# Kernel optimization log

Measured on AMD Instinct MI355X. Metric: run time of the kernel, lower is better.

Reference implementation:

```python
import jax, jax.numpy as jnp
import numpy as np

D_MODEL = 512
TOP_P = 0.25


def setup_inputs() -> dict:
    key = jax.random.key(0)
    ks = jax.random.split(key, 7)
    B, T, D = 4, 4096, D_MODEL
    s = 1.0 / np.sqrt(D)
    return {
        "h": jax.random.normal(ks[0], (B, T, D), dtype=jnp.float32),
        "Wq": jax.random.normal(ks[1], (D, D), dtype=jnp.float32) * s,
        "bq": jnp.zeros((D,), dtype=jnp.float32),
        "Wk": jax.random.normal(ks[2], (D, D), dtype=jnp.float32) * s,
        "bk": jnp.zeros((D,), dtype=jnp.float32),
        "Wv": jax.random.normal(ks[3], (D, D), dtype=jnp.float32) * s,
        "bv": jnp.zeros((D,), dtype=jnp.float32),
    }


def reference(h, Wq, bq, Wk, bk, Wv, bv):
    B, T, D = h.shape
    q = h @ Wq + bq
    k = h @ Wk + bk
    v = h @ Wv + bv
    # [B, T, T] attention scores, scaled by sqrt(d_model)
    scores = jnp.einsum("btd,bsd->bts", q, k) / jnp.sqrt(jnp.asarray(D, h.dtype))
    k_keep = max(1, int(TOP_P * T))
    vals, idx = jax.lax.top_k(scores, k_keep)  # [B, T, k_keep]
    # scatter top-k values back into a -inf-filled mask along the key axis
    bi = jnp.arange(B)[:, None, None]
    ti = jnp.arange(T)[None, :, None]
    mask = jnp.full(scores.shape, -jnp.inf, dtype=scores.dtype)
    mask = mask.at[bi, ti, idx].set(vals)
    attn = jax.nn.softmax(mask, axis=-1)
    out = jnp.einsum("bts,bsd->btd", attn, v)
    return out[:, -1, :]  # only last query's output is used
```

## Files before the change

### kernel.cpp

```cpp
#include <hip/hip_runtime.h>
#include <hip/hip_bf16.h>

#define B 4
#define T 4096
#define D 512
#define KKEEP 1024
#define RSQRT_D 0.044194173824159216f

__device__ __forceinline__ unsigned f2ord(float f) {
    unsigned u = __float_as_uint(f);
    return (u & 0x80000000u) ? ~u : (u | 0x80000000u);
}
__device__ __forceinline__ float ord2f(unsigned o) {
    return __uint_as_float((o & 0x80000000u) ? (o ^ 0x80000000u) : ~o);
}

__global__ void k_zero(float* a, int na, float* o, int no) {
    int i = blockIdx.x * blockDim.x + threadIdx.x;
    if (i < na) a[i] = 0.f;
    if (i < no) o[i] = 0.f;
}

__global__ void k_qlast(const float* __restrict__ h, const float* __restrict__ Wq,
                        const float* __restrict__ bq, float* __restrict__ qlast) {
    int b = blockIdx.x;
    int j = blockIdx.y * 256 + threadIdx.x;
    int d0 = blockIdx.z * 64;
    __shared__ float hs[64];
    const float* hrow = h + ((size_t)b * T + (T - 1)) * D + d0;
    if (threadIdx.x < 64) hs[threadIdx.x] = hrow[threadIdx.x];
    __syncthreads();
    float acc = (blockIdx.z == 0) ? bq[j] : 0.f;
    for (int d = 0; d < 64; ++d) acc += hs[d] * Wq[(size_t)(d0 + d) * D + j];
    atomicAdd(&qlast[b * D + j], acc);
}

__global__ void k_wk(const float* __restrict__ Wk, const float* __restrict__ bk,
                     const float* __restrict__ qlast,
                     float* __restrict__ wvec, float* __restrict__ cvec) {
    int b = blockIdx.x;
    int lane = threadIdx.x & 63;
    int wave = threadIdx.x >> 6;
    const float* qb = qlast + b * D;
    if (blockIdx.y == D / 4) {
        if (wave == 0) {
            float acc = 0.f;
            for (int k = lane; k < D; k += 64) acc += bk[k] * qb[k];
            for (int off = 32; off; off >>= 1) acc += __shfl_down(acc, off);
            if (lane == 0) cvec[b] = acc;
        }
        return;
    }
    int d = blockIdx.y * 4 + wave;
    const float* row = Wk + (size_t)d * D;
    float acc = 0.f;
    for (int k = lane; k < D; k += 64) acc += row[k] * qb[k];
    for (int off = 32; off; off >>= 1) acc += __shfl_down(acc, off);
    if (lane == 0) wvec[b * D + d] = acc;
}

__global__ void k_scores(const float* __restrict__ h, const float* __restrict__ wvec,
                         const float* __restrict__ cvec, float* __restrict__ sc) {
    int b = blockIdx.x;
    __shared__ float ws[D];
    for (int i = threadIdx.x; i < D; i += blockDim.x) ws[i] = wvec[b * D + i];
    __syncthreads();
    int lane = threadIdx.x & 63;
    int wave = threadIdx.x >> 6;
    int s = blockIdx.y * 4 + wave;
    const float4* h4 = (const float4*)(h + ((size_t)b * T + s) * D);
    const float4* w4 = (const float4*)ws;
    float acc = 0.f;
    for (int k = lane; k < D / 4; k += 64) {
        float4 a = h4[k], w = w4[k];
        acc += a.x * w.x + a.y * w.y + a.z * w.z + a.w * w.w;
    }
    for (int off = 32; off; off >>= 1) acc += __shfl_down(acc, off);
    if (lane == 0) sc[b * T + s] = (acc + cvec[b]) * RSQRT_D;
}

__global__ __launch_bounds__(1024) void k_select(const float* __restrict__ sc,
                                                 unsigned* __restrict__ selI,
                                                 float* __restrict__ selW) {
    int b = blockIdx.x;
    int tid = threadIdx.x;
    __shared__ unsigned ordk[T];
    __shared__ int hist[256];
    __shared__ float red[16];
    __shared__ unsigned sI[KKEEP];
    __shared__ float sW[KKEEP];
    __shared__ unsigned tieI[T];
    __shared__ unsigned sh_pv;
    __shared__ int sh_r, sh_cnt, sh_tiecnt;
    __shared__ float sh_max, sh_inv;

    float sv[4];
    float lmax = -INFINITY;
#pragma unroll
    for (int k = 0; k < 4; ++k) {
        int i = tid + k * 1024;
        float v = sc[b * T + i];
        sv[k] = v;
        ordk[i] = f2ord(v);
        lmax = fmaxf(lmax, v);
    }
    for (int off = 32; off; off >>= 1) lmax = fmaxf(lmax, __shfl_down(lmax, off));
    if ((tid & 63) == 0) red[tid >> 6] = lmax;
    __syncthreads();
    if (tid == 0) {
        float m = red[0];
        for (int w = 1; w < 16; ++w) m = fmaxf(m, red[w]);
        sh_max = m; sh_pv = 0; sh_r = KKEEP; sh_cnt = 0; sh_tiecnt = 0;
    }
    __syncthreads();

    for (int p = 24; p >= 0; p -= 8) {
        if (tid < 256) hist[tid] = 0;
        __syncthreads();
        unsigned pv = sh_pv;
#pragma unroll
        for (int k = 0; k < 4; ++k) {
            unsigned key = ordk[tid + k * 1024];
            bool act = (p == 24) || ((key >> (p + 8)) == pv);
            if (act) atomicAdd(&hist[(key >> p) & 255], 1);
        }
        __syncthreads();
        if (tid < 64) {
            int r = sh_r;
            int c0 = hist[tid * 4], c1 = hist[tid * 4 + 1];
            int c2 = hist[tid * 4 + 2], c3 = hist[tid * 4 + 3];
            int s = c0 + c1 + c2 + c3;
            int cum = s;
            for (int off = 1; off < 64; off <<= 1) {
                int v = __shfl_down(cum, off);
                if (tid + off < 64) cum += v;
            }
            int base = cum - s;
            if (base < r && r <= cum) {
                int d, sg;
                if (r <= base + c3)                { d = 3; sg = base; }
                else if (r <= base + c3 + c2)      { d = 2; sg = base + c3; }
                else if (r <= base + c3 + c2 + c1) { d = 1; sg = base + c3 + c2; }
                else                               { d = 0; sg = base + c3 + c2 + c1; }
                sh_pv = (pv << 8) | (unsigned)(tid * 4 + d);
                sh_r = r - sg;
            }
        }
        __syncthreads();
    }

    unsigned vstar = sh_pv;
    int rtie = sh_r;
    float gmax = sh_max;

#pragma unroll
    for (int k = 0; k < 4; ++k) {
        int i = tid + k * 1024;
        unsigned key = ordk[i];
        if (key > vstar) {
            int pos = atomicAdd(&sh_cnt, 1);
            sI[pos] = (unsigned)i;
            sW[pos] = __expf(sv[k] - gmax);
        } else if (key == vstar) {
            int pos = atomicAdd(&sh_tiecnt, 1);
            tieI[pos] = (unsigned)i;
        }
    }
    __syncthreads();

    int tcnt = sh_tiecnt;
    float tw = __expf(ord2f(vstar) - gmax);
    for (int t = tid; t < tcnt; t += 1024) {
        unsigned my = tieI[t];
        int rank = 0;
        for (int o = 0; o < tcnt; ++o) rank += (tieI[o] < my);
        if (rank < rtie) {
            int pos = atomicAdd(&sh_cnt, 1);
            sI[pos] = my;
            sW[pos] = tw;
        }
    }
    __syncthreads();

    float lsum = sW[tid];
    for (int off = 32; off; off >>= 1) lsum += __shfl_down(lsum, off);
    if ((tid & 63) == 0) red[tid >> 6] = lsum;
    __syncthreads();
    if (tid == 0) {
        float s = 0.f;
        for (int w = 0; w < 16; ++w) s += red[w];
        sh_inv = 1.0f / s;
    }
    __syncthreads();
    selI[b * KKEEP + tid] = sI[tid];
    selW[b * KKEEP + tid] = sW[tid] * sh_inv;
}

__global__ __launch_bounds__(512) void k_wsum(const float* __restrict__ h,
                                              const unsigned* __restrict__ selI,
                                              const float* __restrict__ selW,
                                              float* __restrict__ wsum) {
    int b = blockIdx.x;
    int e0 = blockIdx.y * 32;
    int tid = threadIdx.x;
    int g = tid >> 7, l = tid & 127;
    __shared__ float4 red4[512];
    float4 acc = make_float4(0.f, 0.f, 0.f, 0.f);
    for (int e = g; e < 32; e += 4) {
        unsigned s = selI[b * KKEEP + e0 + e];
        float w = selW[b * KKEEP + e0 + e];
        float4 v = ((const float4*)(h + ((size_t)b * T + s) * D))[l];
        acc.x += w * v.x; acc.y += w * v.y; acc.z += w * v.z; acc.w += w * v.w;
    }
    red4[tid] = acc;
    __syncthreads();
    if (tid < 128) {
        float4 a = red4[tid], b1 = red4[tid + 128], c = red4[tid + 256], d4 = red4[tid + 384];
        float* wd = &wsum[b * D + tid * 4];
        atomicAdd(wd + 0, a.x + b1.x + c.x + d4.x);
        atomicAdd(wd + 1, a.y + b1.y + c.y + d4.y);
        atomicAdd(wd + 2, a.z + b1.z + c.z + d4.z);
        atomicAdd(wd + 3, a.w + b1.w + c.w + d4.w);
    }
}

__global__ void k_out(const float* __restrict__ wsum, const float* __restrict__ Wv,
                      const float* __restrict__ bv, float* __restrict__ out) {
    int b = blockIdx.x;
    int j = blockIdx.y * 256 + threadIdx.x;
    int d0 = blockIdx.z * 64;
    __shared__ float ws_[64];
    if (threadIdx.x < 64) ws_[threadIdx.x] = wsum[b * D + d0 + threadIdx.x];
    __syncthreads();
    float acc = (blockIdx.z == 0) ? bv[j] : 0.f;
    for (int d = 0; d < 64; ++d) acc += ws_[d] * Wv[(size_t)(d0 + d) * D + j];
    atomicAdd(&out[b * D + j], acc);
}

extern "C" void kernel_launch(void* const* d_in, const int* in_sizes, int n_in,
                              void* d_out, int out_size, void* d_ws, size_t ws_size,
                              hipStream_t stream) {
    const float* h  = (const float*)d_in[0];
    const float* Wq = (const float*)d_in[1];
    const float* bq = (const float*)d_in[2];
    const float* Wk = (const float*)d_in[3];
    const float* bk = (const float*)d_in[4];
    const float* Wv = (const float*)d_in[5];
    const float* bv = (const float*)d_in[6];
    float* out = (float*)d_out;

    float* ws = (float*)d_ws;
    float* qlast   = ws;
    float* wsum    = ws + 2048;
    float* wvec    = ws + 4096;
    float* cvec    = ws + 6144;
    float* sc      = ws + 6400;
    unsigned* selI = (unsigned*)(ws + 22784);
    float* selW    = ws + 26880;

    k_zero<<<dim3(8), 512, 0, stream>>>(qlast, 4096, out, out_size);
    k_qlast<<<dim3(B, 2, 8), 256, 0, stream>>>(h, Wq, bq, qlast);
    k_wk<<<dim3(B, D / 4 + 1), 256, 0, stream>>>(Wk, bk, qlast, wvec, cvec);
    k_scores<<<dim3(B, T / 4), 256, 0, stream>>>(h, wvec, cvec, sc);
    k_select<<<dim3(B), 1024, 0, stream>>>(sc, selI, selW);
    k_wsum<<<dim3(B, 32), 512, 0, stream>>>(h, selI, selW, wsum);
    k_out<<<dim3(B, 2, 8), 256, 0, stream>>>(wsum, Wv, bv, out);
}
```

Before: 111.4 us.

## Fuse query/key projection prep kernels and replace atomics with partial-sum reduction

The zeroing, last-query projection and Wk-vector kernels are merged into one k_prep kernel with one 1024-thread block per batch, and the 1/sqrt(D) scale is folded into wvec and cvec. k_wsum now writes per-block partial sums instead of doing atomic adds, and k_out reduces those partials and does the full Wv product per block with no atomics. This removes two launches, the zeroing pass and all global atomics. The cost is much less parallelism: the prep stage runs on only 4 blocks and reads Wk with a row-strided, uncoalesced pattern, and k_out drops to 8 blocks.

```diff
diff --git a/kernel.cpp b/kernel.cpp
--- a/kernel.cpp
+++ b/kernel.cpp
@@ -15,48 +15,39 @@
     return __uint_as_float((o & 0x80000000u) ? (o ^ 0x80000000u) : ~o);
 }
 
-__global__ void k_zero(float* a, int na, float* o, int no) {
-    int i = blockIdx.x * blockDim.x + threadIdx.x;
-    if (i < na) a[i] = 0.f;
-    if (i < no) o[i] = 0.f;
-}
-
-__global__ void k_qlast(const float* __restrict__ h, const float* __restrict__ Wq,
-                        const float* __restrict__ bq, float* __restrict__ qlast) {
-    int b = blockIdx.x;
-    int j = blockIdx.y * 256 + threadIdx.x;
-    int d0 = blockIdx.z * 64;
-    __shared__ float hs[64];
-    const float* hrow = h + ((size_t)b * T + (T - 1)) * D + d0;
-    if (threadIdx.x < 64) hs[threadIdx.x] = hrow[threadIdx.x];
-    __syncthreads();
-    float acc = (blockIdx.z == 0) ? bq[j] : 0.f;
-    for (int d = 0; d < 64; ++d) acc += hs[d] * Wq[(size_t)(d0 + d) * D + j];
-    atomicAdd(&qlast[b * D + j], acc);
-}
-
-__global__ void k_wk(const float* __restrict__ Wk, const float* __restrict__ bk,
-                     const float* __restrict__ qlast,
-                     float* __restrict__ wvec, float* __restrict__ cvec) {
-    int b = blockIdx.x;
-    int lane = threadIdx.x & 63;
-    int wave = threadIdx.x >> 6;
-    const float* qb = qlast + b * D;
-    if (blockIdx.y == D / 4) {
-        if (wave == 0) {
-            float acc = 0.f;
-            for (int k = lane; k < D; k += 64) acc += bk[k] * qb[k];
-            for (int off = 32; off; off >>= 1) acc += __shfl_down(acc, off);
-            if (lane == 0) cvec[b] = acc;
-        }
-        return;
-    }
-    int d = blockIdx.y * 4 + wave;
-    const float* row = Wk + (size_t)d * D;
+__global__ __launch_bounds__(1024) void k_prep(const float* __restrict__ h,
+                                               const float* __restrict__ Wq,
+                                               const float* __restrict__ bq,
+                                               const float* __restrict__ Wk,
+                                               const float* __restrict__ bk,
+                                               float* __restrict__ wvec,
+                                               float* __restrict__ cvec) {
+    int b = blockIdx.x, tid = threadIdx.x;
+    int j = tid & 511, half = tid >> 9;
+    int d0 = half * 256;
+    __shared__ float hs[D], q[D], partial[1024];
+    const float* hrow = h + ((size_t)b * T + (T - 1)) * D;
+    if (tid < D) hs[tid] = hrow[tid];
+    __syncthreads();
     float acc = 0.f;
-    for (int k = lane; k < D; k += 64) acc += row[k] * qb[k];
-    for (int off = 32; off; off >>= 1) acc += __shfl_down(acc, off);
-    if (lane == 0) wvec[b * D + d] = acc;
+#pragma unroll 4
+    for (int d = 0; d < 256; ++d) acc += hs[d0 + d] * Wq[(size_t)(d0 + d) * D + j];
+    partial[tid] = acc;
+    __syncthreads();
+    if (tid < D) q[tid] = partial[tid] + partial[tid + 512] + bq[tid];
+    __syncthreads();
+    float acc2 = 0.f;
+#pragma unroll 4
+    for (int k = 0; k < 256; ++k) acc2 += Wk[(size_t)j * D + d0 + k] * q[d0 + k];
+    partial[tid] = acc2;
+    __syncthreads();
+    if (tid < D) wvec[b * D + tid] = (partial[tid] + partial[tid + 512]) * RSQRT_D;
+    if (tid < 64) {
+        float a = 0.f;
+        for (int k = tid; k < D; k += 64) a += bk[k] * q[k];
+        for (int off = 32; off; off >>= 1) a += __shfl_down(a, off);
+        if (tid == 0) cvec[b] = a * RSQRT_D;
+    }
 }
 
 __global__ void k_scores(const float* __restrict__ h, const float* __restrict__ wvec,
@@ -76,7 +67,7 @@
         acc += a.x * w.x + a.y * w.y + a.z * w.z + a.w * w.w;
     }
     for (int off = 32; off; off >>= 1) acc += __shfl_down(acc, off);
-    if (lane == 0) sc[b * T + s] = (acc + cvec[b]) * RSQRT_D;
+    if (lane == 0) sc[b * T + s] = acc + cvec[b];
 }
 
 __global__ __launch_bounds__(1024) void k_select(const float* __restrict__ sc,
@@ -199,11 +190,10 @@
 __global__ __launch_bounds__(512) void k_wsum(const float* __restrict__ h,
                                               const unsigned* __restrict__ selI,
                                               const float* __restrict__ selW,
-                                              float* __restrict__ wsum) {
-    int b = blockIdx.x;
-    int e0 = blockIdx.y * 32;
-    int tid = threadIdx.x;
+                                              float* __restrict__ part) {
+    int b = blockIdx.x, y = blockIdx.y, tid = threadIdx.x;
     int g = tid >> 7, l = tid & 127;
+    int e0 = y * 32;
     __shared__ float4 red4[512];
     float4 acc = make_float4(0.f, 0.f, 0.f, 0.f);
     for (int e = g; e < 32; e += 4) {
@@ -215,26 +205,29 @@
     red4[tid] = acc;
     __syncthreads();
     if (tid < 128) {
-        float4 a = red4[tid], b1 = red4[tid + 128], c = red4[tid + 256], d4 = red4[tid + 384];
-        float* wd = &wsum[b * D + tid * 4];
-        atomicAdd(wd + 0, a.x + b1.x + c.x + d4.x);
-        atomicAdd(wd + 1, a.y + b1.y + c.y + d4.y);
-        atomicAdd(wd + 2, a.z + b1.z + c.z + d4.z);
-        atomicAdd(wd + 3, a.w + b1.w + c.w + d4.w);
-    }
-}
-
-__global__ void k_out(const float* __restrict__ wsum, const float* __restrict__ Wv,
+        float4 a = red4[tid], b4 = red4[tid + 128], c = red4[tid + 256], d4 = red4[tid + 384];
+        float4 r = make_float4(a.x + b4.x + c.x + d4.x, a.y + b4.y + c.y + d4.y,
+                               a.z + b4.z + c.z + d4.z, a.w + b4.w + c.w + d4.w);
+        ((float4*)part)[(b * 32 + y) * 128 + tid] = r;
+    }
+}
+
+__global__ void k_out(const float* __restrict__ part, const float* __restrict__ Wv,
                       const float* __restrict__ bv, float* __restrict__ out) {
-    int b = blockIdx.x;
-    int j = blockIdx.y * 256 + threadIdx.x;
-    int d0 = blockIdx.z * 64;
-    __shared__ float ws_[64];
-    if (threadIdx.x < 64) ws_[threadIdx.x] = wsum[b * D + d0 + threadIdx.x];
-    __syncthreads();
-    float acc = (blockIdx.z == 0) ? bv[j] : 0.f;
-    for (int d = 0; d < 64; ++d) acc += ws_[d] * Wv[(size_t)(d0 + d) * D + j];
-    atomicAdd(&out[b * D + j], acc);
+    int b = blockIdx.x, tid = threadIdx.x;
+    int j = blockIdx.y * 256 + tid;
+    __shared__ float ws_[D];
+    for (int d = tid; d < D; d += 256) {
+        float s = 0.f;
+#pragma unroll 8
+        for (int p = 0; p < 32; ++p) s += part[(size_t)(b * 32 + p) * D + d];
+        ws_[d] = s;
+    }
+    __syncthreads();
+    float acc = bv[j];
+#pragma unroll 4
+    for (int d = 0; d < D; ++d) acc += ws_[d] * Wv[(size_t)d * D + j];
+    out[b * D + j] = acc;
 }
 
 extern "C" void kernel_launch(void* const* d_in, const int* in_sizes, int n_in,
@@ -250,19 +243,16 @@
     float* out = (float*)d_out;
 
     float* ws = (float*)d_ws;
-    float* qlast   = ws;
-    float* wsum    = ws + 2048;
-    float* wvec    = ws + 4096;
-    float* cvec    = ws + 6144;
-    float* sc      = ws + 6400;
-    unsigned* selI = (unsigned*)(ws + 22784);
-    float* selW    = ws + 26880;
-
-    k_zero<<<dim3(8), 512, 0, stream>>>(qlast, 4096, out, out_size);
-    k_qlast<<<dim3(B, 2, 8), 256, 0, stream>>>(h, Wq, bq, qlast);
-    k_wk<<<dim3(B, D / 4 + 1), 256, 0, stream>>>(Wk, bk, qlast, wvec, cvec);
+    float* wvec    = ws;
+    float* cvec    = ws + 2048;
+    float* sc      = ws + 2304;
+    unsigned* selI = (unsigned*)(ws + 18688);
+    float* selW    = ws + 22784;
+    float* part    = ws + 26880;
+
+    k_prep<<<dim3(B), 1024, 0, stream>>>(h, Wq, bq, Wk, bk, wvec, cvec);
     k_scores<<<dim3(B, T / 4), 256, 0, stream>>>(h, wvec, cvec, sc);
     k_select<<<dim3(B), 1024, 0, stream>>>(sc, selI, selW);
-    k_wsum<<<dim3(B, 32), 512, 0, stream>>>(h, selI, selW, wsum);
-    k_out<<<dim3(B, 2, 8), 256, 0, stream>>>(wsum, Wv, bv, out);
-}
+    k_wsum<<<dim3(B, 32), 512, 0, stream>>>(h, selI, selW, part);
+    k_out<<<dim3(B, 2), 256, 0, stream>>>(part, Wv, bv, out);
+}
```

New measurement: 197.3 us. 77.1% more time.
